# Kernel optimization log

Hardware: AMD Instinct MI355X
Metric: run time of the kernel (lower is better)

The kernel has to match this reference:

```python
import jax, jax.numpy as jnp
import numpy as np
import math

N_HEAD = 16
N_EMBD = 1024
BLOCK_SIZE = 2048
B, T = 2, 2048
R = 32.0
MAX_SPAN = float(BLOCK_SIZE)
SPAN_REG = 2e-06
PERIOD_MIN, PERIOD_MAX = 2.0, 4.0
RATIO_MIN, RATIO_MAX = -0.25, 0.25


def setup_inputs() -> dict:
    key = jax.random.key(0)
    ks = jax.random.split(key, 5)
    x = jax.random.normal(ks[0], (B, T, N_EMBD), dtype=jnp.float32)
    # scale weights like nn.Linear init to keep logits sane
    w_attn = jax.random.normal(ks[1], (N_EMBD, 3 * N_EMBD), dtype=jnp.float32) * 0.02
    b_attn = jnp.zeros((3 * N_EMBD,), dtype=jnp.float32)
    w_proj = jax.random.normal(ks[2], (N_EMBD, N_EMBD), dtype=jnp.float32) * 0.02
    b_proj = jnp.zeros((N_EMBD,), dtype=jnp.float32)
    span_params = jnp.zeros((N_HEAD,), dtype=jnp.float32)
    # torch init: period uniform in [2,4] -> logit weight space; ratio 0 -> logit(0.5)=0
    init_period = jax.random.uniform(ks[3], (N_HEAD,), dtype=jnp.float32) * (PERIOD_MAX - PERIOD_MIN) + PERIOD_MIN
    pn = (init_period - PERIOD_MIN) / (PERIOD_MAX - PERIOD_MIN)
    period_weight = jnp.log(pn) - jnp.log1p(-pn)  # logit
    ratio_weight = jnp.zeros((N_HEAD,), dtype=jnp.float32)
    return {"x": x, "w_attn": w_attn, "b_attn": b_attn, "w_proj": w_proj,
            "b_proj": b_proj, "span_params": span_params,
            "period_weight": period_weight, "ratio_weight": ratio_weight}


def _forward(x, w_attn, b_attn, w_proj, b_proj, span_params, period_weight, ratio_weight):
    Bb, Tt, C = x.shape
    D = C // N_HEAD
    qkv = x @ w_attn + b_attn  # [B,T,3C]
    q, k, v = jnp.split(qkv, 3, axis=-1)
    q = q.reshape(Bb, Tt, N_HEAD, D)
    k = k.reshape(Bb, Tt, N_HEAD, D)
    v = v.reshape(Bb, Tt, N_HEAD, D)
    scale = 1.0 / math.sqrt(D)
    att = jnp.einsum('bihd,bjhd->bhij', q, k) * scale  # [B,H,T,T]

    pos = jnp.arange(Tt, dtype=jnp.float32)
    rel = pos[:, None] - pos[None, :]          # [T,T]
    causal = rel >= 0.0
    rel_c = jnp.maximum(rel, 0.0)              # clamp(min=0)

    clamped_spans = jax.nn.sigmoid(span_params) * MAX_SPAN  # [H]
    # span mask: clamp((R - rel + span)/R, 0, 1); non-causal (rel->inf) -> 0
    mask_pos = jnp.where(causal[None, :, :],
                         jnp.clip((R - rel[None, :, :] + clamped_spans[:, None, None]) / R, 0.0, 1.0),
                         0.0)  # [H,T,T]

    period = PERIOD_MIN + (PERIOD_MAX - PERIOD_MIN) * jax.nn.sigmoid(period_weight)  # [H]
    ratio = RATIO_MIN + (RATIO_MAX - RATIO_MIN) * jax.nn.sigmoid(ratio_weight)       # [H]
    amplitude = period / 4.0
    offset = period * ratio
    wave = 0.5 * (jnp.cos(2.0 * math.pi * rel_c[None, :, :] / period[:, None, None]) + 1.0) \
           * amplitude[:, None, None] + 0.5 + offset[:, None, None]
    wave = jnp.clip(wave, 0.0, 1.0)  # [H,T,T]
    loss_terms = 1.0 / period + 2.0 * ratio - 1.0 / PERIOD_MAX - 2.0 * RATIO_MIN  # [H]

    mask = mask_pos * wave  # [H,T,T]

    att = jnp.where(causal[None, None, :, :], att, -jnp.inf)
    att_max = jnp.max(att, axis=-1, keepdims=True)
    att_exp = jnp.exp(att - att_max)
    weighted = att_exp * mask[None]  # [B,H,T,T]
    att = weighted / jnp.sum(weighted, axis=-1, keepdims=True)

    y = jnp.einsum('bhij,bjhd->bihd', att, v).reshape(Bb, Tt, C)
    y = y @ w_proj + b_proj

    span_loss = SPAN_REG * jnp.sum((clamped_spans + R) * loss_terms) / N_HEAD
    return y, span_loss


def reference(x, w_attn, b_attn, w_proj, b_proj, span_params, period_weight, ratio_weight):
    return _forward(x, w_attn, b_attn, w_proj, b_proj, span_params, period_weight, ratio_weight)
```

## Files before the change

### kernel.cpp

```cpp
#include <hip/hip_runtime.h>
#include <math.h>
#include <float.h>

#define NHEAD 16
#define DHEAD 64
#define SEQT  2048
#define NB    2
#define CEMB  1024
#define C3    3072

typedef __attribute__((ext_vector_type(8))) short  s16x8;
typedef __attribute__((ext_vector_type(4))) short  s16x4;
typedef __attribute__((ext_vector_type(8))) unsigned short u16x8;
typedef __attribute__((ext_vector_type(4))) unsigned short u16x4;
typedef __attribute__((ext_vector_type(4))) float  f32x4;

__device__ __forceinline__ float sigmoidf_(float x) { return 1.0f / (1.0f + expf(-x)); }

__device__ __forceinline__ unsigned short f2b(float f) {
    __bf16 b = (__bf16)f;
    return __builtin_bit_cast(unsigned short, b);
}

__device__ __forceinline__ void gload16(const void* g, void* l) {
    __builtin_amdgcn_global_load_lds(
        (const __attribute__((address_space(1))) void*)g,
        (__attribute__((address_space(3))) void*)l, 16, 0, 0);
}

__global__ __launch_bounds__(256) void convert_bf16(const float* __restrict__ s,
                                                    unsigned short* __restrict__ d)
{
    int i = (blockIdx.x * 256 + threadIdx.x) * 4;
    float4 v = *reinterpret_cast<const float4*>(s + i);
    u16x4 o = { f2b(v.x), f2b(v.y), f2b(v.z), f2b(v.w) };
    *reinterpret_cast<u16x4*>(d + i) = o;
}

__global__ __launch_bounds__(256) void transpose_convert(
    const float* __restrict__ src, unsigned short* __restrict__ dst,
    int rows, int cols)
{
    __shared__ float t[64][65];
    const int tid = threadIdx.x;
    const int c0 = blockIdx.x * 64, r0 = blockIdx.y * 64;
    const int tr = tid >> 4, tc = tid & 15;
#pragma unroll
    for (int l = 0; l < 4; ++l) {
        int r = l * 16 + tr;
        float4 vv = *reinterpret_cast<const float4*>(
            &src[(size_t)(r0 + r) * cols + c0 + tc * 4]);
        t[r][tc * 4 + 0] = vv.x; t[r][tc * 4 + 1] = vv.y;
        t[r][tc * 4 + 2] = vv.z; t[r][tc * 4 + 3] = vv.w;
    }
    __syncthreads();
#pragma unroll
    for (int l = 0; l < 4; ++l) {
        int n = l * 16 + tr;
        u16x4 o4 = { f2b(t[tc * 4 + 0][n]), f2b(t[tc * 4 + 1][n]),
                     f2b(t[tc * 4 + 2][n]), f2b(t[tc * 4 + 3][n]) };
        *reinterpret_cast<u16x4*>(&dst[(size_t)(c0 + n) * rows + r0 + tc * 4]) = o4;
    }
}

__global__ void build_ltab(const float* __restrict__ sp, const float* __restrict__ pw,
                           const float* __restrict__ rw, float* __restrict__ ltab)
{
    const int h = blockIdx.x;
    const float span   = sigmoidf_(sp[h]) * 2048.0f;
    const float period = 2.0f + 2.0f * sigmoidf_(pw[h]);
    const float ratio  = -0.25f + 0.5f * sigmoidf_(rw[h]);
    const float amp    = period * 0.25f;
    const float off    = period * ratio;
    for (int rel = threadIdx.x; rel < SEQT; rel += blockDim.x) {
        float mp = fminf(fmaxf((32.0f - (float)rel + span) * 0.03125f, 0.0f), 1.0f);
        float wv = 0.5f * (cosf(6.283185307179586f * (float)rel / period) + 1.0f) * amp
                   + 0.5f + off;
        wv = fminf(fmaxf(wv, 0.0f), 1.0f);
        float m = mp * wv;
        ltab[h * SEQT + rel] = (m > 0.0f) ? (log2f(m) - 8.0f) : -1e30f;
    }
}

template<int N_, int MODE>
__global__ __launch_bounds__(256) void mfma_gemm(
    const unsigned short* __restrict__ A, const unsigned short* __restrict__ Wt,
    const float* __restrict__ bias, float* __restrict__ outf,
    unsigned short* __restrict__ qo, unsigned short* __restrict__ ko,
    unsigned short* __restrict__ vo)
{
    __shared__ unsigned short As[128 * 64];
    __shared__ unsigned short Bs[128 * 64];
    char* AsB = (char*)As;
    char* BsB = (char*)Bs;

    const int tid  = threadIdx.x;
    const int lane = tid & 63;
    const int wid  = tid >> 6;
    const int wm   = wid >> 1, wn = wid & 1;
    const int g    = lane >> 4, l15 = lane & 15;
    const int m0   = blockIdx.y * 128, n0 = blockIdx.x * 128;

    const int srow = lane >> 3;
    const int skel = 8 * ((lane & 7) ^ srow);
    const int swz  = (lane & 7) << 4;

    f32x4 acc[4][4];
#pragma unroll
    for (int i = 0; i < 4; ++i)
#pragma unroll
        for (int j = 0; j < 4; ++j) acc[i][j] = (f32x4){0.f, 0.f, 0.f, 0.f};

    for (int kt = 0; kt < 16; ++kt) {
        const int k0 = kt * 64;
#pragma unroll
        for (int it = 0; it < 4; ++it) {
            int cc = wid * 4 + it;
            int row = cc * 8 + srow;
            gload16(A  + (size_t)(m0 + row) * 1024 + k0 + skel, AsB + cc * 1024);
            gload16(Wt + (size_t)(n0 + row) * 1024 + k0 + skel, BsB + cc * 1024);
        }
        __syncthreads();
#pragma unroll
        for (int kk = 0; kk < 2; ++kk) {
            s16x8 af[4], bfr[4];
#pragma unroll
            for (int mf = 0; mf < 4; ++mf) {
                int m = wm * 64 + mf * 16 + l15;
                af[mf] = *reinterpret_cast<const s16x8*>(
                    AsB + m * 128 + ((kk * 64 + g * 16) ^ swz));
            }
#pragma unroll
            for (int nf = 0; nf < 4; ++nf) {
                int n = wn * 64 + nf * 16 + l15;
                bfr[nf] = *reinterpret_cast<const s16x8*>(
                    BsB + n * 128 + ((kk * 64 + g * 16) ^ swz));
            }
#pragma unroll
            for (int mf = 0; mf < 4; ++mf)
#pragma unroll
                for (int nf = 0; nf < 4; ++nf)
                    acc[mf][nf] = __builtin_amdgcn_mfma_f32_16x16x32_bf16(
                        af[mf], bfr[nf], acc[mf][nf], 0, 0, 0);
        }
        __syncthreads();
    }

#pragma unroll
    for (int mf = 0; mf < 4; ++mf)
#pragma unroll
        for (int nf = 0; nf < 4; ++nf) {
            const int n = n0 + wn * 64 + nf * 16 + l15;
            const int mb = m0 + wm * 64 + mf * 16 + 4 * g;
            const float bs = bias[n];
            if (MODE == 0) {
                const int which = n >> 10;
                const int cc = n & 1023;
                const int hh = cc >> 6, dd = cc & 63;
                const int t0 = mb & (SEQT - 1);
                const int bb = mb >> 11;
                if (which == 2) {
                    u16x4 pk;
#pragma unroll
                    for (int r = 0; r < 4; ++r) pk[r] = f2b(acc[mf][nf][r] + bs);
                    *reinterpret_cast<u16x4*>(
                        &vo[(((size_t)bb * NHEAD + hh) * DHEAD + dd) * SEQT + t0]) = pk;
                } else {
                    unsigned short* dst = (which == 0) ? qo : ko;
#pragma unroll
                    for (int r = 0; r < 4; ++r)
                        dst[(((size_t)bb * NHEAD + hh) * SEQT + t0 + r) * DHEAD + dd] =
                            f2b(acc[mf][nf][r] + bs);
                }
            } else {
#pragma unroll
                for (int r = 0; r < 4; ++r)
                    outf[(size_t)(mb + r) * N_ + n] = acc[mf][nf][r] + bs;
            }
        }
}

__global__ __launch_bounds__(256) void attn_mfma(
    const unsigned short* __restrict__ q, const unsigned short* __restrict__ k,
    const unsigned short* __restrict__ vt, const float* __restrict__ ltab,
    const float* __restrict__ span_p, unsigned short* __restrict__ y)
{
    __shared__ unsigned short Ks[64 * 64];
    __shared__ unsigned short Vs[64 * 64];

    const int tid  = threadIdx.x;
    const int lane = tid & 63;
    const int w    = tid >> 6;
    const int g    = lane >> 4, l15 = lane & 15;
    const int q0   = blockIdx.x * 64;
    const int bh   = blockIdx.y, b = bh >> 4, h = bh & 15;

    const float span = sigmoidf_(span_p[h]) * 2048.0f;
    const float thr  = 32.0f + span;
    const float* lt  = ltab + h * SEQT;

    const size_t base = (size_t)bh * SEQT * DHEAD;
    const unsigned short* qb  = q  + base;
    const unsigned short* kb  = k  + base;
    const unsigned short* vtb = vt + base;

    s16x8 qa[2];
    {
        const char* qrow = (const char*)(qb + (size_t)(q0 + 16 * w + l15) * DHEAD);
        qa[0] = *reinterpret_cast<const s16x8*>(qrow + g * 16);
        qa[1] = *reinterpret_cast<const s16x8*>(qrow + 64 + g * 16);
    }

    f32x4 oa[4];
#pragma unroll
    for (int i = 0; i < 4; ++i) oa[i] = (f32x4){0.f, 0.f, 0.f, 0.f};
    float lrp = 0.f;

    const int srow = lane >> 3;
    const int skel = 8 * ((lane & 7) ^ srow);
    const int swz  = (lane & 7) << 4;
    const int qrel = q0 + 16 * w + l15;
    const float SCL = 0.18033688f;

    for (int j0 = 0; j0 <= q0; j0 += 64) {
        if ((float)(q0 - j0 - 63) >= thr) continue;

        __syncthreads();
#pragma unroll
        for (int it = 0; it < 2; ++it) {
            int cc = w * 2 + it;
            gload16(kb  + (size_t)(j0 + cc * 8 + srow) * DHEAD + skel,
                    (char*)Ks + cc * 1024);
            gload16(vtb + (size_t)(cc * 8 + srow) * SEQT + j0 + skel,
                    (char*)Vs + cc * 1024);
        }
        __syncthreads();

        f32x4 st[4];
#pragma unroll
        for (int nf = 0; nf < 4; ++nf) st[nf] = (f32x4){0.f, 0.f, 0.f, 0.f};
#pragma unroll
        for (int kk = 0; kk < 2; ++kk)
#pragma unroll
            for (int nf = 0; nf < 4; ++nf) {
                int c = nf * 16 + l15;
                s16x8 kf = *reinterpret_cast<const s16x8*>(
                    (char*)Ks + c * 128 + ((kk * 64 + g * 16) ^ swz));
                st[nf] = __builtin_amdgcn_mfma_f32_16x16x32_bf16(kf, qa[kk], st[nf], 0, 0, 0);
            }

        const int r0 = qrel - j0;
        float pv[4][4];
#pragma unroll
        for (int nf = 0; nf < 4; ++nf)
#pragma unroll
            for (int r = 0; r < 4; ++r) {
                int rel = r0 - 16 * nf - 4 * g - r;
                float p = 0.f;
                if (rel >= 0) p = exp2f(fmaf(st[nf][r], SCL, lt[rel]));
                pv[nf][r] = p;
                lrp += p;
            }

        s16x8 pa[2];
#pragma unroll
        for (int kk = 0; kk < 2; ++kk)
#pragma unroll
            for (int half = 0; half < 2; ++half)
#pragma unroll
                for (int r = 0; r < 4; ++r)
                    pa[kk][half * 4 + r] = (short)f2b(pv[kk * 2 + half][r]);

#pragma unroll
        for (int kk = 0; kk < 2; ++kk)
#pragma unroll
            for (int nfd = 0; nfd < 4; ++nfd) {
                const char* vrow = (const char*)Vs + (nfd * 16 + l15) * 128;
                int o1 = (kk * 64 + g * 8) ^ swz;
                int o2 = (kk * 64 + g * 8 + 32) ^ swz;
                s16x4 lo = *reinterpret_cast<const s16x4*>(vrow + o1);
                s16x4 hi = *reinterpret_cast<const s16x4*>(vrow + o2);
                s16x8 vf;
#pragma unroll
                for (int e = 0; e < 4; ++e) { vf[e] = lo[e]; vf[4 + e] = hi[e]; }
                oa[nfd] = __builtin_amdgcn_mfma_f32_16x16x32_bf16(pa[kk], vf, oa[nfd], 0, 0, 0);
            }
    }

    float lf = lrp;
    lf += __shfl_xor(lf, 16, 64);
    lf += __shfl_xor(lf, 32, 64);

#pragma unroll
    for (int r = 0; r < 4; ++r) {
        int src = (lane & 48) | (4 * g + r);
        float inv = 1.0f / __shfl(lf, src, 64);
        int gr = q0 + 16 * w + 4 * g + r;
#pragma unroll
        for (int nfd = 0; nfd < 4; ++nfd)
            y[((size_t)b * SEQT + gr) * CEMB + h * 64 + nfd * 16 + l15] =
                f2b(oa[nfd][r] * inv);
    }
}

__global__ void span_loss_kernel(const float* __restrict__ sp,
                                 const float* __restrict__ pw,
                                 const float* __restrict__ rw,
                                 float* __restrict__ out)
{
    int lane = threadIdx.x;
    float val = 0.f;
    if (lane < NHEAD) {
        float span   = sigmoidf_(sp[lane]) * 2048.0f;
        float period = 2.0f + 2.0f * sigmoidf_(pw[lane]);
        float ratio  = -0.25f + 0.5f * sigmoidf_(rw[lane]);
        float ltm = 1.0f / period + 2.0f * ratio - 0.25f + 0.5f;
        val = (span + 32.0f) * ltm;
    }
#pragma unroll
    for (int o = 1; o < 16; o <<= 1) val += __shfl_xor(val, o, 64);
    if (lane == 0) out[0] = 2e-6f * val / 16.0f;
}

extern "C" void kernel_launch(void* const* d_in, const int* in_sizes, int n_in,
                              void* d_out, int out_size, void* d_ws, size_t ws_size,
                              hipStream_t stream)
{
    const float* x        = (const float*)d_in[0];
    const float* w_attn   = (const float*)d_in[1];
    const float* b_attn   = (const float*)d_in[2];
    const float* w_proj   = (const float*)d_in[3];
    const float* b_proj   = (const float*)d_in[4];
    const float* span_p   = (const float*)d_in[5];
    const float* period_w = (const float*)d_in[6];
    const float* ratio_w  = (const float*)d_in[7];

    char* ws = (char*)d_ws;
    unsigned short* xb  = (unsigned short*)(ws);
    unsigned short* wT  = (unsigned short*)(ws + ((size_t)8  << 20));
    unsigned short* wpT = (unsigned short*)(ws + ((size_t)14 << 20));
    unsigned short* qb  = (unsigned short*)(ws + ((size_t)16 << 20));
    unsigned short* kb  = (unsigned short*)(ws + ((size_t)24 << 20));
    unsigned short* vt  = (unsigned short*)(ws + ((size_t)32 << 20));
    float*          lt  = (float*)         (ws + ((size_t)40 << 20));
    unsigned short* y1  = xb;

    float* out = (float*)d_out;
    const size_t PLANE = (size_t)NB * SEQT * CEMB;

    convert_bf16<<<4096, 256, 0, stream>>>(x, xb);
    transpose_convert<<<dim3(C3 / 64, CEMB / 64), 256, 0, stream>>>(w_attn, wT, CEMB, C3);
    transpose_convert<<<dim3(CEMB / 64, CEMB / 64), 256, 0, stream>>>(w_proj, wpT, CEMB, CEMB);
    build_ltab<<<NHEAD, 256, 0, stream>>>(span_p, period_w, ratio_w, lt);

    mfma_gemm<C3, 0><<<dim3(C3 / 128, (NB * SEQT) / 128), 256, 0, stream>>>(
        xb, wT, b_attn, nullptr, qb, kb, vt);

    attn_mfma<<<dim3(SEQT / 64, NB * NHEAD), 256, 0, stream>>>(
        qb, kb, vt, lt, span_p, y1);

    mfma_gemm<CEMB, 1><<<dim3(CEMB / 128, (NB * SEQT) / 128), 256, 0, stream>>>(
        y1, wpT, b_proj, out, nullptr, nullptr, nullptr);

    span_loss_kernel<<<1, 64, 0, stream>>>(span_p, period_w, ratio_w, out + PLANE);
}
```

Baseline: 239.8 us.

## Double-buffer K/V tiles, precompute span start, and remap blocks across XCDs

The attention kernel now holds two LDS buffers for K and V. It issues the global load of the next tile before computing on the current one, and needs one barrier per iteration instead of two. The first tile that passes the span mask is computed once up front rather than by skipping tiles inside the loop. The block index is remapped so that all query tiles of a given batch-head land on the same XCD, which is meant to improve L2 reuse of K and V. The cost is twice the LDS use, which may lower occupancy, and the remap assumes a grid of 32 query tiles by 32 batch-heads.

```diff
diff --git a/kernel.cpp b/kernel.cpp
--- a/kernel.cpp
+++ b/kernel.cpp
@@ -185,15 +185,21 @@
     const unsigned short* __restrict__ vt, const float* __restrict__ ltab,
     const float* __restrict__ span_p, unsigned short* __restrict__ y)
 {
-    __shared__ unsigned short Ks[64 * 64];
-    __shared__ unsigned short Vs[64 * 64];
+    __shared__ unsigned short Ks[2][64 * 64];
+    __shared__ unsigned short Vs[2][64 * 64];
 
     const int tid  = threadIdx.x;
     const int lane = tid & 63;
     const int w    = tid >> 6;
     const int g    = lane >> 4, l15 = lane & 15;
-    const int q0   = blockIdx.x * 64;
-    const int bh   = blockIdx.y, b = bh >> 4, h = bh & 15;
+
+    const int wgid = blockIdx.x + gridDim.x * blockIdx.y;
+    const int xcd  = wgid & 7;
+    const int idx  = wgid >> 3;
+    const int bh   = (idx >> 5) * 8 + xcd;
+    const int qt   = idx & 31;
+    const int q0   = qt * 64;
+    const int b    = bh >> 4, h = bh & 15;
 
     const float span = sigmoidf_(span_p[h]) * 2048.0f;
     const float thr  = 32.0f + span;
@@ -222,19 +228,29 @@
     const int qrel = q0 + 16 * w + l15;
     const float SCL = 0.18033688f;
 
-    for (int j0 = 0; j0 <= q0; j0 += 64) {
-        if ((float)(q0 - j0 - 63) >= thr) continue;
-
-        __syncthreads();
+    int jstart = 0;
+    {
+        float lim = (float)(q0 - 63) - thr;
+        if (lim >= 0.0f) jstart = (((int)lim) >> 6) * 64 + 64;
+    }
+
+    auto STAGE = [&](int bsel, int j0s) {
 #pragma unroll
         for (int it = 0; it < 2; ++it) {
             int cc = w * 2 + it;
-            gload16(kb  + (size_t)(j0 + cc * 8 + srow) * DHEAD + skel,
-                    (char*)Ks + cc * 1024);
-            gload16(vtb + (size_t)(cc * 8 + srow) * SEQT + j0 + skel,
-                    (char*)Vs + cc * 1024);
+            gload16(kb  + (size_t)(j0s + cc * 8 + srow) * DHEAD + skel,
+                    (char*)Ks[bsel] + cc * 1024);
+            gload16(vtb + (size_t)(cc * 8 + srow) * SEQT + j0s + skel,
+                    (char*)Vs[bsel] + cc * 1024);
         }
-        __syncthreads();
+    };
+
+    STAGE(0, jstart);
+    __syncthreads();
+    int cur = 0;
+
+    for (int j0 = jstart; j0 <= q0; j0 += 64) {
+        if (j0 + 64 <= q0) STAGE(cur ^ 1, j0 + 64);
 
         f32x4 st[4];
 #pragma unroll
@@ -245,12 +261,12 @@
             for (int nf = 0; nf < 4; ++nf) {
                 int c = nf * 16 + l15;
                 s16x8 kf = *reinterpret_cast<const s16x8*>(
-                    (char*)Ks + c * 128 + ((kk * 64 + g * 16) ^ swz));
+                    (char*)Ks[cur] + c * 128 + ((kk * 64 + g * 16) ^ swz));
                 st[nf] = __builtin_amdgcn_mfma_f32_16x16x32_bf16(kf, qa[kk], st[nf], 0, 0, 0);
             }
 
         const int r0 = qrel - j0;
-        float pv[4][4];
+        float pvv[4][4];
 #pragma unroll
         for (int nf = 0; nf < 4; ++nf)
 #pragma unroll
@@ -258,7 +274,7 @@
                 int rel = r0 - 16 * nf - 4 * g - r;
                 float p = 0.f;
                 if (rel >= 0) p = exp2f(fmaf(st[nf][r], SCL, lt[rel]));
-                pv[nf][r] = p;
+                pvv[nf][r] = p;
                 lrp += p;
             }
 
@@ -269,13 +285,13 @@
             for (int half = 0; half < 2; ++half)
 #pragma unroll
                 for (int r = 0; r < 4; ++r)
-                    pa[kk][half * 4 + r] = (short)f2b(pv[kk * 2 + half][r]);
+                    pa[kk][half * 4 + r] = (short)f2b(pvv[kk * 2 + half][r]);
 
 #pragma unroll
         for (int kk = 0; kk < 2; ++kk)
 #pragma unroll
             for (int nfd = 0; nfd < 4; ++nfd) {
-                const char* vrow = (const char*)Vs + (nfd * 16 + l15) * 128;
+                const char* vrow = (const char*)Vs[cur] + (nfd * 16 + l15) * 128;
                 int o1 = (kk * 64 + g * 8) ^ swz;
                 int o2 = (kk * 64 + g * 8 + 32) ^ swz;
                 s16x4 lo = *reinterpret_cast<const s16x4*>(vrow + o1);
@@ -285,6 +301,9 @@
                 for (int e = 0; e < 4; ++e) { vf[e] = lo[e]; vf[4 + e] = hi[e]; }
                 oa[nfd] = __builtin_amdgcn_mfma_f32_16x16x32_bf16(pa[kk], vf, oa[nfd], 0, 0, 0);
             }
+
+        __syncthreads();
+        cur ^= 1;
     }
 
     float lf = lrp;
```

New measurement: 229.7 us. 1.04x faster.
